# Kernel optimization log

Hardware: AMD Instinct MI355X
Metric: run time of the kernel (lower is better)

Reference implementation:

```python
import jax, jax.numpy as jnp
import numpy as np

N_NODES = 100000
IN_CH = 128
OUT_CH = 128
N_EDGES = 625000


def setup_inputs() -> dict:
    key = jax.random.key(0)
    k1, k2, k3, k4 = jax.random.split(key, 4)
    x = jax.random.normal(k1, (N_NODES, IN_CH), dtype=jnp.float32)
    edge_index = jax.random.randint(k2, (2, N_EDGES), 0, N_NODES, dtype=jnp.int64)
    # nn.Linear params (kaiming-uniform-ish init not needed for correctness; use scaled normal)
    W = jax.random.normal(k3, (OUT_CH, IN_CH), dtype=jnp.float32) / np.sqrt(IN_CH)
    b = jax.random.normal(k4, (OUT_CH,), dtype=jnp.float32) * 0.01
    return {"x": x, "edge_index": edge_index, "W": W, "b": b}


def reference(x, edge_index, W, b):
    # Linear: [N, in] @ [in, out] + [out]
    x_transformed = jnp.einsum("ni,oi->no", x, W) + b  # [N, out]
    src = edge_index[0]  # [E]
    dst = edge_index[1]  # [E]
    # scatter-add: neighbor_features[dst] += x_transformed[src]
    neighbor_features = jax.ops.segment_sum(
        x_transformed[src], dst, num_segments=x.shape[0]
    )  # [N, out]
    return neighbor_features + x_transformed
```

## Files before the change

kernel.cpp:

```cpp
#include <hip/hip_runtime.h>

constexpr int NN = 100000;
constexpr int CH = 128;
constexpr int NE = 625000;
constexpr int GEMM_BLOCKS = (NN + 127) / 128;
constexpr int BUCKET_BLOCKS = 256;
constexpr int EDGES_PER_BLOCK = (NE + BUCKET_BLOCKS - 1) / BUCKET_BLOCKS;
constexpr int NB = 196;
constexpr int CAP = 4096;
constexpr int WCONV_BLOCKS = 16;

typedef __bf16 bf16x8 __attribute__((ext_vector_type(8)));
typedef __bf16 bf16x4 __attribute__((ext_vector_type(4)));
typedef float  f32x4  __attribute__((ext_vector_type(4)));

__device__ __forceinline__ float bflo(uint u) { return __uint_as_float(u << 16); }
__device__ __forceinline__ float bfhi(uint u) { return __uint_as_float(u & 0xffff0000u); }

__device__ __forceinline__ void async_copy16(const void* g, void* l) {
    __builtin_amdgcn_global_load_lds(
        (const __attribute__((address_space(1))) unsigned int*)(uintptr_t)g,
        (__attribute__((address_space(3))) unsigned int*)(uintptr_t)l,
        16, 0, 0);
}

__global__ __launch_bounds__(256) void prep_kernel(
    int* __restrict__ gcursor, const float* __restrict__ W, __bf16* __restrict__ Wb)
{
    if (blockIdx.x == 0) {
        gcursor[threadIdx.x] = threadIdx.x * CAP;
        return;
    }
    int i = (blockIdx.x - 1) * 256 + threadIdx.x;
    int ch = i >> 5;
    int k0 = (i & 31) * 4;
    float4 v = reinterpret_cast<const float4*>(W)[i];
    bf16x4 h = {(__bf16)v.x, (__bf16)v.y, (__bf16)v.z, (__bf16)v.w};
    *reinterpret_cast<bf16x4*>(&Wb[ch * 128 + (k0 ^ ((ch & 7) << 3))]) = h;
}

__global__ __launch_bounds__(512) void gemm_bucket_kernel(
    const float* __restrict__ x, const __bf16* __restrict__ Wb,
    const float* __restrict__ b, __bf16* __restrict__ xt,
    const int* __restrict__ ei, int* __restrict__ gcursor, int2* __restrict__ pairs)
{
    __shared__ __bf16 wlds[128 * 128];
    const int tid = threadIdx.x;

    if (blockIdx.x < BUCKET_BLOCKS) {
        int* lhist = (int*)wlds;
        int* lbase = lhist + 256;
        const int e0 = blockIdx.x * EDGES_PER_BLOCK;
        const int myN = min(NE - e0, EDGES_PER_BLOCK);
        if (tid < 256) lhist[tid] = 0;
        __syncthreads();
        for (int i = tid; i < myN; i += 512) {
            int dst = ei[NE + e0 + i];
            atomicAdd(&lhist[dst >> 9], 1);
        }
        __syncthreads();
        if (tid < 256) {
            int c = lhist[tid];
            if (c) lbase[tid] = atomicAdd(&gcursor[tid], c);
            lhist[tid] = 0;
        }
        __syncthreads();
        for (int i = tid; i < myN; i += 512) {
            int src = ei[e0 + i];
            int dst = ei[NE + e0 + i];
            int bin = dst >> 9;
            int r = atomicAdd(&lhist[bin], 1);
            pairs[lbase[bin] + r] = make_int2(src, dst);
        }
        return;
    }

    const int lane = tid & 63;
    const int w    = tid >> 6;
    const int lm = lane & 15;
    const int lk = lane >> 4;
    const int row = (blockIdx.x - BUCKET_BLOCKS) * 128 + w * 16 + lm;
    const int rc  = row < NN ? row : NN - 1;

    const float* xrow = x + (size_t)rc * CH;
    float4 xr[8];
    #pragma unroll
    for (int ks = 0; ks < 4; ++ks) {
        const float4* p = reinterpret_cast<const float4*>(xrow + ks * 32 + lk * 8);
        xr[ks * 2]     = p[0];
        xr[ks * 2 + 1] = p[1];
    }

    const bf16x8* Wb8 = reinterpret_cast<const bf16x8*>(Wb);
    #pragma unroll
    for (int it = 0; it < 4; ++it) {
        async_copy16(Wb8 + it * 512 + tid,
                     (char*)wlds + (size_t)(it * 512 + w * 64) * 16);
    }

    bf16x8 bfrag[4];
    #pragma unroll
    for (int ks = 0; ks < 4; ++ks) {
        float4 u = xr[ks * 2], v = xr[ks * 2 + 1];
        bfrag[ks][0] = (__bf16)u.x; bfrag[ks][1] = (__bf16)u.y;
        bfrag[ks][2] = (__bf16)u.z; bfrag[ks][3] = (__bf16)u.w;
        bfrag[ks][4] = (__bf16)v.x; bfrag[ks][5] = (__bf16)v.y;
        bfrag[ks][6] = (__bf16)v.z; bfrag[ks][7] = (__bf16)v.w;
    }

    __syncthreads();

    const float4* B4 = reinterpret_cast<const float4*>(b);
    const int swz = (lm & 7) << 3;

    #pragma unroll
    for (int t = 0; t < 8; ++t) {
        const int ch = t * 16 + lm;
        float4 bv = B4[t * 4 + lk];
        f32x4 acc = {bv.x, bv.y, bv.z, bv.w};
        #pragma unroll
        for (int ks = 0; ks < 4; ++ks) {
            bf16x8 afrag = *reinterpret_cast<const bf16x8*>(
                &wlds[ch * 128 + ((ks * 32 + lk * 8) ^ swz)]);
            acc = __builtin_amdgcn_mfma_f32_16x16x32_bf16(afrag, bfrag[ks], acc, 0, 0, 0);
        }
        if (row < NN) {
            const int c0 = t * 16 + lk * 4;
            bf16x4 hv = {(__bf16)acc[0], (__bf16)acc[1], (__bf16)acc[2], (__bf16)acc[3]};
            *reinterpret_cast<bf16x4*>(&xt[(size_t)row * CH + c0]) = hv;
        }
    }
}

__global__ __launch_bounds__(256) void place2_kernel(
    const int* __restrict__ gcursor, const int2* __restrict__ pairs,
    int* __restrict__ srcs, int* __restrict__ offs)
{
    __shared__ int cntb[256];
    __shared__ int cnt512[512];
    __shared__ int pref[512];
    __shared__ int dense_base;
    const int tid = threadIdx.x;
    const int bkt = blockIdx.x;

    int c = gcursor[tid] - tid * CAP;
    cntb[tid] = c;
    __syncthreads();
    for (int off = 1; off < 256; off <<= 1) {
        int u = (tid >= off) ? cntb[tid - off] : 0;
        __syncthreads();
        cntb[tid] += u;
        __syncthreads();
    }
    if (tid == bkt) dense_base = cntb[tid] - c;
    if (bkt == 0 && tid == 255) offs[NN] = cntb[255];
    __syncthreads();

    const int n = gcursor[bkt] - bkt * CAP;
    const int2* P = pairs + (size_t)bkt * CAP;

    cnt512[tid] = 0; cnt512[tid + 256] = 0;
    __syncthreads();
    for (int i = tid; i < n; i += 256)
        atomicAdd(&cnt512[P[i].y & 511], 1);
    __syncthreads();

    int c0 = cnt512[2 * tid], c1 = cnt512[2 * tid + 1];
    int ps = c0 + c1;
    cntb[tid] = ps;
    __syncthreads();
    for (int off = 1; off < 256; off <<= 1) {
        int u = (tid >= off) ? cntb[tid - off] : 0;
        __syncthreads();
        cntb[tid] += u;
        __syncthreads();
    }
    int ex = cntb[tid] - ps;
    pref[2 * tid] = ex;
    pref[2 * tid + 1] = ex + c0;

    {
        int d0 = bkt * 512 + 2 * tid;
        if (d0 < NN)     offs[d0]     = dense_base + ex;
        if (d0 + 1 < NN) offs[d0 + 1] = dense_base + ex + c0;
    }
    __syncthreads();

    for (int i = tid; i < n; i += 256) {
        int2 p = P[i];
        int pos = atomicAdd(&pref[p.y & 511], 1);
        srcs[dense_base + pos] = p.x;
    }
}

__global__ __launch_bounds__(256) void gather_kernel(
    const uint4* __restrict__ xtu4,
    const int* __restrict__ offs, const int* __restrict__ srcs,
    float* __restrict__ out)
{
    const int gid  = blockIdx.x * 256 + threadIdx.x;
    const int lane = threadIdx.x & 63;
    const int q    = lane >> 4;
    const int l16  = lane & 15;
    const int node = ((gid >> 6) << 2) + q;
    const int nd   = node < NN ? node : NN - 1;

    uint4 own = xtu4[(size_t)nd * 16 + l16];
    float a0 = bflo(own.x), a1 = bfhi(own.x);
    float a2 = bflo(own.y), a3 = bfhi(own.y);
    float a4 = bflo(own.z), a5 = bfhi(own.z);
    float a6 = bflo(own.w), a7 = bfhi(own.w);

    int beg = offs[nd];
    const int end = offs[nd + 1];

    while (beg < end) {
        const int n = min(end - beg, 16);
        const int myidx = (l16 < n) ? srcs[beg + l16] : 0;
        int k = 0;
        for (; k + 1 < n; k += 2) {
            int s0 = __shfl(myidx, (q << 4) + k);
            int s1 = __shfl(myidx, (q << 4) + k + 1);
            uint4 h0 = xtu4[(size_t)s0 * 16 + l16];
            uint4 h1 = xtu4[(size_t)s1 * 16 + l16];
            a0 += bflo(h0.x); a1 += bfhi(h0.x);
            a2 += bflo(h0.y); a3 += bfhi(h0.y);
            a4 += bflo(h0.z); a5 += bfhi(h0.z);
            a6 += bflo(h0.w); a7 += bfhi(h0.w);
            a0 += bflo(h1.x); a1 += bfhi(h1.x);
            a2 += bflo(h1.y); a3 += bfhi(h1.y);
            a4 += bflo(h1.z); a5 += bfhi(h1.z);
            a6 += bflo(h1.w); a7 += bfhi(h1.w);
        }
        if (k < n) {
            int s0 = __shfl(myidx, (q << 4) + k);
            uint4 h0 = xtu4[(size_t)s0 * 16 + l16];
            a0 += bflo(h0.x); a1 += bfhi(h0.x);
            a2 += bflo(h0.y); a3 += bfhi(h0.y);
            a4 += bflo(h0.z); a5 += bfhi(h0.z);
            a6 += bflo(h0.w); a7 += bfhi(h0.w);
        }
        beg += n;
    }

    if (node < NN) {
        float4* o4 = reinterpret_cast<float4*>(out) + (size_t)node * 32 + l16 * 2;
        o4[0] = make_float4(a0, a1, a2, a3);
        o4[1] = make_float4(a4, a5, a6, a7);
    }
}

extern "C" void kernel_launch(void* const* d_in, const int* in_sizes, int n_in,
                              void* d_out, int out_size, void* d_ws, size_t ws_size,
                              hipStream_t stream) {
    const float* x  = (const float*)d_in[0];
    const int*   ei = (const int*)d_in[1];
    const float* W  = (const float*)d_in[2];
    const float* b  = (const float*)d_in[3];
    float* out = (float*)d_out;

    __bf16* xt     = (__bf16*)d_ws;
    int2*   pairs  = (int2*)(xt + (size_t)NN * CH);
    int*    srcs   = (int*)(pairs + (size_t)256 * CAP);
    int*    offs   = srcs + NE;
    int*    gcur   = offs + NN + 1;
    __bf16* Wb     = (__bf16*)(gcur + 256);

    prep_kernel<<<1 + WCONV_BLOCKS, 256, 0, stream>>>(gcur, W, Wb);
    gemm_bucket_kernel<<<BUCKET_BLOCKS + GEMM_BLOCKS, 512, 0, stream>>>(
        x, Wb, b, xt, ei, gcur, pairs);
    place2_kernel<<<NB, 256, 0, stream>>>(gcur, pairs, srcs, offs);
    const int gwaves = (NN + 3) / 4;
    gather_kernel<<<(gwaves * 64 + 255) / 256, 256, 0, stream>>>(
        (const uint4*)xt, offs, srcs, out);
}
```

Measured before the change: 82.11 us.

## Split GEMM tiles across bucket and place kernels to overlap work

Moves the GEMM tile code into a shared device helper. Part of the GEMM blocks (558 of them) stay in the bucketing kernel, and the rest move into the place kernel, which now runs with 512 threads per block. This balances load and fills the GPU while the small 196-block place phase runs. It also adds nontemporal loads for x and nontemporal stores for the output to cut cache pollution. The place logic is adapted to 512 threads, with guards so only the first 256 threads do the scans.

```diff
diff --git a/kernel.cpp b/kernel.cpp
--- a/kernel.cpp
+++ b/kernel.cpp
@@ -4,6 +4,8 @@
 constexpr int CH = 128;
 constexpr int NE = 625000;
 constexpr int GEMM_BLOCKS = (NN + 127) / 128;
+constexpr int SPLIT1 = 558;
+constexpr int SPLIT2 = GEMM_BLOCKS - SPLIT1;
 constexpr int BUCKET_BLOCKS = 256;
 constexpr int EDGES_PER_BLOCK = (NE + BUCKET_BLOCKS - 1) / BUCKET_BLOCKS;
 constexpr int NB = 196;
@@ -39,73 +41,40 @@
     *reinterpret_cast<bf16x4*>(&Wb[ch * 128 + (k0 ^ ((ch & 7) << 3))]) = h;
 }
 
-__global__ __launch_bounds__(512) void gemm_bucket_kernel(
-    const float* __restrict__ x, const __bf16* __restrict__ Wb,
+__device__ __forceinline__ void gemm_tile(
+    const float* __restrict__ x, const bf16x8* __restrict__ Wb8,
     const float* __restrict__ b, __bf16* __restrict__ xt,
-    const int* __restrict__ ei, int* __restrict__ gcursor, int2* __restrict__ pairs)
-{
-    __shared__ __bf16 wlds[128 * 128];
-    const int tid = threadIdx.x;
-
-    if (blockIdx.x < BUCKET_BLOCKS) {
-        int* lhist = (int*)wlds;
-        int* lbase = lhist + 256;
-        const int e0 = blockIdx.x * EDGES_PER_BLOCK;
-        const int myN = min(NE - e0, EDGES_PER_BLOCK);
-        if (tid < 256) lhist[tid] = 0;
-        __syncthreads();
-        for (int i = tid; i < myN; i += 512) {
-            int dst = ei[NE + e0 + i];
-            atomicAdd(&lhist[dst >> 9], 1);
-        }
-        __syncthreads();
-        if (tid < 256) {
-            int c = lhist[tid];
-            if (c) lbase[tid] = atomicAdd(&gcursor[tid], c);
-            lhist[tid] = 0;
-        }
-        __syncthreads();
-        for (int i = tid; i < myN; i += 512) {
-            int src = ei[e0 + i];
-            int dst = ei[NE + e0 + i];
-            int bin = dst >> 9;
-            int r = atomicAdd(&lhist[bin], 1);
-            pairs[lbase[bin] + r] = make_int2(src, dst);
-        }
-        return;
-    }
-
+    __bf16* wlds, int tid, int row_base)
+{
     const int lane = tid & 63;
     const int w    = tid >> 6;
     const int lm = lane & 15;
     const int lk = lane >> 4;
-    const int row = (blockIdx.x - BUCKET_BLOCKS) * 128 + w * 16 + lm;
+    const int row = row_base + w * 16 + lm;
     const int rc  = row < NN ? row : NN - 1;
 
     const float* xrow = x + (size_t)rc * CH;
-    float4 xr[8];
+    f32x4 xr[8];
     #pragma unroll
     for (int ks = 0; ks < 4; ++ks) {
-        const float4* p = reinterpret_cast<const float4*>(xrow + ks * 32 + lk * 8);
-        xr[ks * 2]     = p[0];
-        xr[ks * 2 + 1] = p[1];
-    }
-
-    const bf16x8* Wb8 = reinterpret_cast<const bf16x8*>(Wb);
+        const f32x4* p = reinterpret_cast<const f32x4*>(xrow + ks * 32 + lk * 8);
+        xr[ks * 2]     = __builtin_nontemporal_load(p);
+        xr[ks * 2 + 1] = __builtin_nontemporal_load(p + 1);
+    }
+
     #pragma unroll
-    for (int it = 0; it < 4; ++it) {
+    for (int it = 0; it < 4; ++it)
         async_copy16(Wb8 + it * 512 + tid,
                      (char*)wlds + (size_t)(it * 512 + w * 64) * 16);
-    }
 
     bf16x8 bfrag[4];
     #pragma unroll
     for (int ks = 0; ks < 4; ++ks) {
-        float4 u = xr[ks * 2], v = xr[ks * 2 + 1];
-        bfrag[ks][0] = (__bf16)u.x; bfrag[ks][1] = (__bf16)u.y;
-        bfrag[ks][2] = (__bf16)u.z; bfrag[ks][3] = (__bf16)u.w;
-        bfrag[ks][4] = (__bf16)v.x; bfrag[ks][5] = (__bf16)v.y;
-        bfrag[ks][6] = (__bf16)v.z; bfrag[ks][7] = (__bf16)v.w;
+        f32x4 u = xr[ks * 2], v = xr[ks * 2 + 1];
+        bfrag[ks][0] = (__bf16)u[0]; bfrag[ks][1] = (__bf16)u[1];
+        bfrag[ks][2] = (__bf16)u[2]; bfrag[ks][3] = (__bf16)u[3];
+        bfrag[ks][4] = (__bf16)v[0]; bfrag[ks][5] = (__bf16)v[1];
+        bfrag[ks][6] = (__bf16)v[2]; bfrag[ks][7] = (__bf16)v[3];
     }
 
     __syncthreads();
@@ -132,65 +101,119 @@
     }
 }
 
-__global__ __launch_bounds__(256) void place2_kernel(
+__global__ __launch_bounds__(512) void gemm_bucket_kernel(
+    const float* __restrict__ x, const __bf16* __restrict__ Wb,
+    const float* __restrict__ b, __bf16* __restrict__ xt,
+    const int* __restrict__ ei, int* __restrict__ gcursor, int2* __restrict__ pairs)
+{
+    __shared__ __bf16 wlds[128 * 128];
+    const int tid = threadIdx.x;
+
+    if (blockIdx.x < BUCKET_BLOCKS) {
+        int* lhist = (int*)wlds;
+        int* lbase = lhist + 256;
+        const int e0 = blockIdx.x * EDGES_PER_BLOCK;
+        const int myN = min(NE - e0, EDGES_PER_BLOCK);
+        if (tid < 256) lhist[tid] = 0;
+        __syncthreads();
+        for (int i = tid; i < myN; i += 512) {
+            int dst = ei[NE + e0 + i];
+            atomicAdd(&lhist[dst >> 9], 1);
+        }
+        __syncthreads();
+        if (tid < 256) {
+            int c = lhist[tid];
+            if (c) lbase[tid] = atomicAdd(&gcursor[tid], c);
+            lhist[tid] = 0;
+        }
+        __syncthreads();
+        for (int i = tid; i < myN; i += 512) {
+            int src = ei[e0 + i];
+            int dst = ei[NE + e0 + i];
+            int bin = dst >> 9;
+            int r = atomicAdd(&lhist[bin], 1);
+            pairs[lbase[bin] + r] = make_int2(src, dst);
+        }
+        return;
+    }
+
+    gemm_tile(x, reinterpret_cast<const bf16x8*>(Wb), b, xt, wlds, tid,
+              (blockIdx.x - BUCKET_BLOCKS) * 128);
+}
+
+__global__ __launch_bounds__(512) void gemm_place_kernel(
+    const float* __restrict__ x, const __bf16* __restrict__ Wb,
+    const float* __restrict__ b, __bf16* __restrict__ xt,
     const int* __restrict__ gcursor, const int2* __restrict__ pairs,
     int* __restrict__ srcs, int* __restrict__ offs)
 {
-    __shared__ int cntb[256];
-    __shared__ int cnt512[512];
-    __shared__ int pref[512];
-    __shared__ int dense_base;
+    __shared__ __bf16 wlds[128 * 128];
     const int tid = threadIdx.x;
-    const int bkt = blockIdx.x;
-
-    int c = gcursor[tid] - tid * CAP;
-    cntb[tid] = c;
-    __syncthreads();
-    for (int off = 1; off < 256; off <<= 1) {
-        int u = (tid >= off) ? cntb[tid - off] : 0;
-        __syncthreads();
-        cntb[tid] += u;
-        __syncthreads();
-    }
-    if (tid == bkt) dense_base = cntb[tid] - c;
-    if (bkt == 0 && tid == 255) offs[NN] = cntb[255];
-    __syncthreads();
-
-    const int n = gcursor[bkt] - bkt * CAP;
-    const int2* P = pairs + (size_t)bkt * CAP;
-
-    cnt512[tid] = 0; cnt512[tid + 256] = 0;
-    __syncthreads();
-    for (int i = tid; i < n; i += 256)
-        atomicAdd(&cnt512[P[i].y & 511], 1);
-    __syncthreads();
-
-    int c0 = cnt512[2 * tid], c1 = cnt512[2 * tid + 1];
-    int ps = c0 + c1;
-    cntb[tid] = ps;
-    __syncthreads();
-    for (int off = 1; off < 256; off <<= 1) {
-        int u = (tid >= off) ? cntb[tid - off] : 0;
-        __syncthreads();
-        cntb[tid] += u;
-        __syncthreads();
-    }
-    int ex = cntb[tid] - ps;
-    pref[2 * tid] = ex;
-    pref[2 * tid + 1] = ex + c0;
-
-    {
-        int d0 = bkt * 512 + 2 * tid;
-        if (d0 < NN)     offs[d0]     = dense_base + ex;
-        if (d0 + 1 < NN) offs[d0 + 1] = dense_base + ex + c0;
-    }
-    __syncthreads();
-
-    for (int i = tid; i < n; i += 256) {
-        int2 p = P[i];
-        int pos = atomicAdd(&pref[p.y & 511], 1);
-        srcs[dense_base + pos] = p.x;
-    }
+
+    if (blockIdx.x < NB) {
+        int* cntb   = (int*)wlds;
+        int* cnt512 = cntb + 256;
+        int* pref   = cnt512 + 512;
+        int* dbase  = pref + 512;
+        const int bkt = blockIdx.x;
+
+        int c = 0;
+        if (tid < 256) { c = gcursor[tid] - tid * CAP; cntb[tid] = c; }
+        __syncthreads();
+        for (int off = 1; off < 256; off <<= 1) {
+            int u = (tid < 256 && tid >= off) ? cntb[tid - off] : 0;
+            __syncthreads();
+            if (tid < 256) cntb[tid] += u;
+            __syncthreads();
+        }
+        if (tid == bkt) dbase[0] = cntb[bkt] - c;
+        if (bkt == 0 && tid == 255) offs[NN] = cntb[255];
+        __syncthreads();
+
+        const int n = gcursor[bkt] - bkt * CAP;
+        const int2* P = pairs + (size_t)bkt * CAP;
+
+        cnt512[tid] = 0;
+        __syncthreads();
+        for (int i = tid; i < n; i += 512)
+            atomicAdd(&cnt512[P[i].y & 511], 1);
+        __syncthreads();
+
+        int c0 = 0, c1 = 0, ps = 0;
+        if (tid < 256) {
+            c0 = cnt512[2 * tid]; c1 = cnt512[2 * tid + 1];
+            ps = c0 + c1;
+            cntb[tid] = ps;
+        }
+        __syncthreads();
+        for (int off = 1; off < 256; off <<= 1) {
+            int u = (tid < 256 && tid >= off) ? cntb[tid - off] : 0;
+            __syncthreads();
+            if (tid < 256) cntb[tid] += u;
+            __syncthreads();
+        }
+        if (tid < 256) {
+            int ex = cntb[tid] - ps;
+            pref[2 * tid] = ex;
+            pref[2 * tid + 1] = ex + c0;
+            int db = dbase[0];
+            int d0 = bkt * 512 + 2 * tid;
+            if (d0 < NN)     offs[d0]     = db + ex;
+            if (d0 + 1 < NN) offs[d0 + 1] = db + ex + c0;
+        }
+        __syncthreads();
+
+        const int db = dbase[0];
+        for (int i = tid; i < n; i += 512) {
+            int2 p = P[i];
+            int pos = atomicAdd(&pref[p.y & 511], 1);
+            srcs[db + pos] = p.x;
+        }
+        return;
+    }
+
+    gemm_tile(x, reinterpret_cast<const bf16x8*>(Wb), b, xt, wlds, tid,
+              (blockIdx.x - NB + SPLIT1) * 128);
 }
 
 __global__ __launch_bounds__(256) void gather_kernel(
@@ -244,9 +267,11 @@
     }
 
     if (node < NN) {
-        float4* o4 = reinterpret_cast<float4*>(out) + (size_t)node * 32 + l16 * 2;
-        o4[0] = make_float4(a0, a1, a2, a3);
-        o4[1] = make_float4(a4, a5, a6, a7);
+        f32x4 v0 = {a0, a1, a2, a3};
+        f32x4 v1 = {a4, a5, a6, a7};
+        f32x4* o4 = reinterpret_cast<f32x4*>(out) + (size_t)node * 32 + l16 * 2;
+        __builtin_nontemporal_store(v0, o4);
+        __builtin_nontemporal_store(v1, o4 + 1);
     }
 }
 
@@ -267,9 +292,10 @@
     __bf16* Wb     = (__bf16*)(gcur + 256);
 
     prep_kernel<<<1 + WCONV_BLOCKS, 256, 0, stream>>>(gcur, W, Wb);
-    gemm_bucket_kernel<<<BUCKET_BLOCKS + GEMM_BLOCKS, 512, 0, stream>>>(
+    gemm_bucket_kernel<<<BUCKET_BLOCKS + SPLIT1, 512, 0, stream>>>(
         x, Wb, b, xt, ei, gcur, pairs);
-    place2_kernel<<<NB, 256, 0, stream>>>(gcur, pairs, srcs, offs);
+    gemm_place_kernel<<<NB + SPLIT2, 512, 0, stream>>>(
+        x, Wb, b, xt, gcur, pairs, srcs, offs);
     const int gwaves = (NN + 3) / 4;
     gather_kernel<<<(gwaves * 64 + 255) / 256, 256, 0, stream>>>(
         (const uint4*)xt, offs, srcs, out);
```

Measured after the change: 85.13 us. 1.04x slower.
